# Kernel optimization log

Measured on AMD Instinct MI355X. Metric: run time of the kernel, lower is better.

Reference implementation:

```python
import jax, jax.numpy as jnp
import numpy as np

N, E, G = 8000, 100000, 256
H, C = 4, 128
ATOM_F = 92
L = 5


def _ln(x, g, b, eps=1e-5):
    mu = jnp.mean(x, axis=-1, keepdims=True)
    var = jnp.mean((x - mu) ** 2, axis=-1, keepdims=True)
    return (x - mu) * jax.lax.rsqrt(var + eps) * g + b


def setup_inputs() -> dict:
    key = jax.random.key(0)
    ks = iter(jax.random.split(key, 64))
    p = lambda shape: jax.random.normal(next(ks), shape, jnp.float32) * 0.05
    inp = {}
    inp['x'] = jax.random.normal(next(ks), (N, ATOM_F), jnp.float32)
    inp['edge_attr'] = jax.random.uniform(next(ks), (E,), jnp.float32)
    inp['edge_index'] = jax.random.randint(next(ks), (2, E), 0, N)
    inp['batch'] = jnp.sort(jax.random.randint(next(ks), (N,), 0, G))
    # atom embedding + rbf MLP
    inp['W_atom'] = p((ATOM_F, C)); inp['b_atom'] = jnp.zeros((C,))
    inp['W_rbf1'] = p((C, C)); inp['b_rbf1'] = jnp.zeros((C,))
    inp['W_rbf2'] = p((C, C)); inp['b_rbf2'] = jnp.zeros((C,))
    # 5 MatformerConv layers, params stacked on leading L dim
    inp['Wq'] = p((L, C, H * C)); inp['bq'] = jnp.zeros((L, H * C))
    inp['Wk'] = p((L, C, H * C)); inp['bk'] = jnp.zeros((L, H * C))
    inp['Wv'] = p((L, C, H * C)); inp['bv'] = jnp.zeros((L, H * C))
    inp['We'] = p((L, C, H * C))  # lin_edge has no bias
    inp['Wc'] = p((L, H * C, C)); inp['bc'] = jnp.zeros((L, C))
    inp['Wm'] = p((L, 3 * C, 3 * C)); inp['bm'] = jnp.zeros((L, 3 * C))
    inp['Wmsg'] = p((L, 3 * C, C)); inp['bmsg'] = jnp.zeros((L, C))
    inp['lnA_g'] = jnp.ones((L, 3 * C)); inp['lnA_b'] = jnp.zeros((L, 3 * C))
    inp['lnM_g'] = jnp.ones((L, C)); inp['lnM_b'] = jnp.zeros((L, C))
    inp['bn_g'] = jnp.ones((L, C)); inp['bn_b'] = jnp.zeros((L, C))
    inp['W_fc'] = p((C, C)); inp['b_fc'] = jnp.zeros((C,))
    return inp


def reference(x, edge_attr, edge_index, batch, W_atom, b_atom, W_rbf1, b_rbf1,
              W_rbf2, b_rbf2, Wq, bq, Wk, bk, Wv, bv, We, Wc, bc, Wm, bm,
              Wmsg, bmsg, lnA_g, lnA_b, lnM_g, lnM_b, bn_g, bn_b, W_fc, b_fc):
    n = x.shape[0]
    e_n = edge_attr.shape[0]
    src, dst = edge_index[0], edge_index[1]  # message flows src -> dst
    h = x @ W_atom + b_atom  # [N, C]
    # RBFExpansion(vmin=0, vmax=8, bins=128): gamma = 1/lengthscale
    centers = jnp.linspace(0.0, 8.0, C)
    gamma = (C - 1) / 8.0
    rbf = jnp.exp(-gamma * (edge_attr[:, None] - centers) ** 2)  # [E, C]
    ef = jax.nn.softplus(rbf @ W_rbf1 + b_rbf1) @ W_rbf2 + b_rbf2  # [E, C]
    scale = 1.0 / np.sqrt(3.0 * C).astype(np.float32)
    for l in range(L):
        q = (h @ Wq[l] + bq[l]).reshape(n, H, C)
        k = (h @ Wk[l] + bk[l]).reshape(n, H, C)
        v = (h @ Wv[l] + bv[l]).reshape(n, H, C)
        e = (ef @ We[l]).reshape(e_n, H, C)
        qi, ki, vi = q[dst], k[dst], v[dst]
        kj, vj = k[src], v[src]
        qc = jnp.concatenate([qi, qi, qi], axis=-1)           # [E, H, 3C]
        kc = jnp.concatenate([ki, kj, e], axis=-1)            # [E, H, 3C]
        alpha = qc * kc * scale
        gate = jax.nn.sigmoid(_ln(alpha, lnA_g[l], lnA_b[l]))
        m = jnp.concatenate([vi, vj, e], axis=-1) @ Wm[l] + bm[l]
        m = m * gate                                          # [E, H, 3C]
        m = _ln(m @ Wmsg[l] + bmsg[l], lnM_g[l], lnM_b[l])    # [E, H, C]
        agg = jax.ops.segment_sum(m.reshape(e_n, H * C), dst, num_segments=N)
        o = agg @ Wc[l] + bc[l]                               # [N, C]
        mu = jnp.mean(o, axis=0)
        var = jnp.mean((o - mu) ** 2, axis=0)                 # BatchNorm1d (train mode)
        o = (o - mu) * jax.lax.rsqrt(var + 1e-5) * bn_g[l] + bn_b[l]
        h = jax.nn.silu(o)
    counts = jax.ops.segment_sum(jnp.ones((n,), jnp.float32), batch, num_segments=G)
    pooled = jax.ops.segment_sum(h, batch, num_segments=G) / jnp.maximum(counts, 1.0)[:, None]
    return jax.nn.silu(pooled @ W_fc + b_fc)  # [G, 128]
```

## Files before the change

kernel.cpp:

```cpp
#include <hip/hip_runtime.h>
#include <math.h>

#define NN 8000
#define NE 100000
#define NG 256
#define CC 128
#define NH 4
#define HD 512
#define C3 384
#define HC3 1536
#define NL 5
#define AF 92
#define TE 16
#define TE2 32
#define NEB (NE/TE2)
#define SCALE 0.05103103630798288f

typedef __attribute__((ext_vector_type(8))) __bf16 bf16x8;
typedef __attribute__((ext_vector_type(4))) float f32x4;
typedef __attribute__((ext_vector_type(16))) float f32x16;
typedef __attribute__((ext_vector_type(8))) unsigned short us8;

static __device__ __forceinline__ bf16x8 ldbf8(const unsigned short* p){
  us8 v = *reinterpret_cast<const us8*>(p);
  return __builtin_bit_cast(bf16x8, v);
}
static __device__ __forceinline__ unsigned short f2bf(float f){
  unsigned int u = __builtin_bit_cast(unsigned int, f);
  u += 0x7FFFu + ((u >> 16) & 1u);
  return (unsigned short)(u >> 16);
}
static __device__ __forceinline__ float bf2f(unsigned short u){
  unsigned int x = ((unsigned int)u) << 16;
  return __builtin_bit_cast(float, x);
}
static __device__ __forceinline__ unsigned int packbf(float a, float b){
  return (unsigned int)f2bf(a) | ((unsigned int)f2bf(b) << 16);
}
static __device__ __forceinline__ float sigf(float x){ return 1.0f/(1.0f+__expf(-x)); }
static __device__ __forceinline__ float siluf(float x){ return x/(1.0f+__expf(-x)); }
static __device__ __forceinline__ float softplusf(float x){
  return x > 0.0f ? x + __logf(1.0f+__expf(-x)) : __logf(1.0f+__expf(x));
}
static __device__ __forceinline__ int permJ(int P){
  int tt = P >> 5;
  int r  = P & 31;
  int w  = tt / 3, part = tt - 3*w;
  return part*128 + w*32 + r;
}

__global__ void k_hist(const int* __restrict__ dstI, int* __restrict__ cnt){
  int i = blockIdx.x*256 + threadIdx.x;
  if (i < NE) atomicAdd(&cnt[dstI[i]], 1);
}
__global__ __launch_bounds__(1024)
void k_scan(const int* __restrict__ cnt, int* __restrict__ offs, int* __restrict__ cursor){
  __shared__ int a_s[1024], b_s[1024];
  int t = threadIdx.x;
  int base = t*8;
  int v[8]; int s = 0;
  #pragma unroll
  for (int j = 0; j < 8; ++j){
    int c = (base+j < NN) ? cnt[base+j] : 0;
    v[j] = s; s += c;
  }
  a_s[t] = s; __syncthreads();
  int* srcp = a_s; int* dstp = b_s;
  for (int off = 1; off < 1024; off <<= 1){
    int x = srcp[t];
    if (t >= off) x += srcp[t-off];
    dstp[t] = x; __syncthreads();
    int* tmp = srcp; srcp = dstp; dstp = tmp;
  }
  int excl = (t == 0) ? 0 : srcp[t-1];
  #pragma unroll
  for (int j = 0; j < 8; ++j){
    if (base+j < NN){ offs[base+j] = excl + v[j]; cursor[base+j] = excl + v[j]; }
  }
}
__global__ void k_scatter(const int* __restrict__ dstI, int* __restrict__ cursor,
                          int* __restrict__ sperm){
  int i = blockIdx.x*256 + threadIdx.x;
  if (i < NE){
    int d = dstI[i];
    int pos = atomicAdd(&cursor[d], 1);
    sperm[pos] = i;
  }
}
__global__ void k_meta(const int* __restrict__ sperm, const int* __restrict__ srcI,
                       const int* __restrict__ dstI, int* __restrict__ ssrc,
                       int* __restrict__ sdst){
  int i = blockIdx.x*256 + threadIdx.x;
  if (i < NE){ int e = sperm[i]; ssrc[i] = srcI[e]; sdst[i] = dstI[e]; }
}
__global__ void k_permute_ef(const int* __restrict__ sperm,
                             const uint2* __restrict__ ef_in, uint2* __restrict__ ef_out){
  int i = blockIdx.x*256 + threadIdx.x;
  if (i < NE*32){
    int row = i >> 5, p = i & 31;
    ef_out[(size_t)row*32 + p] = ef_in[(size_t)sperm[row]*32 + p];
  }
}

__global__ void k_prep_we(const float* __restrict__ We, unsigned short* __restrict__ WeA){
  size_t i = (size_t)blockIdx.x*256 + threadIdx.x;
  if (i >= (size_t)NL*NH*CC*CC) return;
  int k = i & 127; int r = (i>>7)&127; int hh = (i>>14)&3; int li = (int)(i>>16);
  WeA[i] = f2bf(We[((size_t)li*CC + k)*HD + hh*CC + r]);
}
__global__ void k_prep_wv(const float* __restrict__ Wm, unsigned short* __restrict__ WvA){
  size_t i = (size_t)blockIdx.x*256 + threadIdx.x;
  if (i >= (size_t)NL*768*CC) return;
  int k = i & 127; int R = (int)((i>>7) % 768); int li = (int)(i / (768*CC));
  int P = (R < C3) ? R : R - C3;
  int j = permJ(P);
  float val = (R < C3) ? Wm[((size_t)li*C3 + k)*C3 + j]
                       : Wm[((size_t)li*C3 + 128 + k)*C3 + j];
  WvA[i] = f2bf(val);
}
__global__ void k_prep_wg(const float* __restrict__ Wmsg, unsigned short* __restrict__ WgA){
  size_t i = (size_t)blockIdx.x*256 + threadIdx.x;
  if (i >= (size_t)NL*CC*C3) return;
  int P = (int)(i % C3); int c = (int)((i / C3) % CC); int li = (int)(i / ((size_t)CC*C3));
  WgA[i] = f2bf(Wmsg[((size_t)li*C3 + permJ(P))*CC + c]);
}
__global__ __launch_bounds__(128)
void k_prep_wf(const float* __restrict__ We, const float* __restrict__ Wm,
               unsigned short* __restrict__ WfA){
  int b = blockIdx.x;
  int P = b % C3; int hh = (b / C3) & 3; int li = b / (C3*NH);
  int o = permJ(P);
  __shared__ float wcol[CC];
  int t = threadIdx.x;
  wcol[t] = Wm[((size_t)li*C3 + 256 + t)*C3 + o];
  __syncthreads();
  const float* werow = We + ((size_t)li*CC + t)*HD + hh*CC;
  float acc = 0.f;
  #pragma unroll 4
  for (int c = 0; c < CC; ++c) acc += werow[c] * wcol[c];
  WfA[(((size_t)li*NH + hh)*C3 + P)*CC + t] = f2bf(acc);
}
__global__ void k_prep_wqkv(const float* __restrict__ Wq, const float* __restrict__ Wk,
                            const float* __restrict__ Wv, unsigned short* __restrict__ WA){
  size_t i = (size_t)blockIdx.x*256 + threadIdx.x;
  if (i >= (size_t)NL*1536*CC) return;
  int k = i & 127; int m = (int)((i>>7) % 1536); int li = (int)(i / ((size_t)1536*CC));
  const float* W = (m < 512) ? Wq : (m < 1024) ? Wk : Wv;
  int mm = m & 511;
  WA[i] = f2bf(W[((size_t)li*CC + k)*HD + mm]);
}
__global__ void k_prep_wc(const float* __restrict__ Wc, unsigned short* __restrict__ WcA){
  size_t i = (size_t)blockIdx.x*256 + threadIdx.x;
  if (i >= (size_t)NL*CC*HD) return;
  int k = (int)(i & 511); int r = (int)((i>>9) & 127); int li = (int)(i >> 16);
  WcA[i] = f2bf(Wc[((size_t)li*HD + k)*CC + r]);
}

__global__ __launch_bounds__(128)
void k_stem(const float* __restrict__ x, const float* __restrict__ W,
            const float* __restrict__ b, float* __restrict__ h,
            unsigned short* __restrict__ h_bf){
  __shared__ float xs[8][AF];
  int n0 = blockIdx.x*8;
  int t = threadIdx.x;
  for (int i = t; i < 8*AF; i += 128){ xs[i/AF][i%AF] = x[(size_t)n0*AF + i]; }
  __syncthreads();
  float acc[8] = {};
  for (int f = 0; f < AF; ++f){
    float w = W[f*CC + t];
    #pragma unroll
    for (int n = 0; n < 8; ++n) acc[n] += xs[n][f]*w;
  }
  float bb = b[t];
  #pragma unroll
  for (int n = 0; n < 8; ++n){
    float hv = acc[n] + bb;
    h[(size_t)(n0+n)*CC + t] = hv;
    h_bf[(size_t)(n0+n)*CC + t] = f2bf(hv);
  }
}

__global__ __launch_bounds__(128)
void k_rbf(const float* __restrict__ ea, const float* __restrict__ W1, const float* __restrict__ b1,
           const float* __restrict__ W2, const float* __restrict__ b2,
           unsigned short* __restrict__ ef){
  __shared__ __align__(16) float rs[8][CC];
  __shared__ __align__(16) float ss[8][CC];
  __shared__ float dv[8];
  int e0 = blockIdx.x*8; int t = threadIdx.x;
  if (t < 8) dv[t] = ea[e0 + t];
  __syncthreads();
  float center = (8.0f/127.0f) * (float)t;
  const float gamma = 15.875f;
  #pragma unroll
  for (int n = 0; n < 8; ++n){ float d = dv[n] - center; rs[n][t] = __expf(-gamma*d*d); }
  __syncthreads();
  {
    float acc[8] = {};
    for (int c0 = 0; c0 < CC; c0 += 4){
      float w0 = W1[(c0+0)*CC+t], w1 = W1[(c0+1)*CC+t], w2 = W1[(c0+2)*CC+t], w3 = W1[(c0+3)*CC+t];
      #pragma unroll
      for (int n = 0; n < 8; ++n){
        float4 r4 = *(const float4*)&rs[n][c0];
        acc[n] += r4.x*w0 + r4.y*w1 + r4.z*w2 + r4.w*w3;
      }
    }
    float bb = b1[t];
    #pragma unroll
    for (int n = 0; n < 8; ++n) ss[n][t] = softplusf(acc[n] + bb);
  }
  __syncthreads();
  {
    float acc[8] = {};
    for (int c0 = 0; c0 < CC; c0 += 4){
      float w0 = W2[(c0+0)*CC+t], w1 = W2[(c0+1)*CC+t], w2 = W2[(c0+2)*CC+t], w3 = W2[(c0+3)*CC+t];
      #pragma unroll
      for (int n = 0; n < 8; ++n){
        float4 r4 = *(const float4*)&ss[n][c0];
        acc[n] += r4.x*w0 + r4.y*w1 + r4.z*w2 + r4.w*w3;
      }
    }
    float bb = b2[t];
    #pragma unroll
    for (int n = 0; n < 8; ++n) ef[(size_t)(e0+n)*CC + t] = f2bf(acc[n] + bb);
  }
}

__global__ __launch_bounds__(256)
void k_qkv_mfma(const unsigned short* __restrict__ h_bf,
                const unsigned short* __restrict__ WA,
                const float* __restrict__ bq_, const float* __restrict__ bk_,
                const float* __restrict__ bv_,
                unsigned short* __restrict__ qo, unsigned short* __restrict__ ko,
                unsigned short* __restrict__ vo){
  const int t = threadIdx.x;
  const int w = t >> 6, lane = t & 63;
  const int col = lane & 31, hi = lane >> 5;
  const int node = blockIdx.x * 32 + col;
  const int yw = blockIdx.y;

  const unsigned short* hrow = h_bf + (size_t)node*CC + hi*8;
  bf16x8 bfr[8];
  #pragma unroll
  for (int kc = 0; kc < 8; ++kc) bfr[kc] = ldbf8(hrow + kc*16);

  const float* bias = (yw == 0) ? bq_ : (yw == 1) ? bk_ : bv_;
  unsigned short* outp = (yw == 0) ? qo : (yw == 1) ? ko : vo;
  const unsigned short* Wbase = WA + (size_t)yw*512*CC;

  #pragma unroll
  for (int mt = 0; mt < 4; ++mt){
    f32x16 acc;
    #pragma unroll
    for (int i = 0; i < 16; ++i) acc[i] = 0.f;
    const unsigned short* arow = Wbase + (size_t)(w*128 + mt*32 + col)*CC + hi*8;
    #pragma unroll
    for (int kc = 0; kc < 8; ++kc)
      acc = __builtin_amdgcn_mfma_f32_32x32x16_bf16(ldbf8(arow + kc*16), bfr[kc], acc, 0,0,0);
    #pragma unroll
    for (int g = 0; g < 4; ++g){
      int cb = w*128 + mt*32 + 8*g + 4*hi;
      float4 bb = *(const float4*)(bias + cb);
      uint2 uv;
      uv.x = packbf(acc[4*g+0]+bb.x, acc[4*g+1]+bb.y);
      uv.y = packbf(acc[4*g+2]+bb.z, acc[4*g+3]+bb.w);
      *(uint2*)(outp + (size_t)node*HD + cb) = uv;
    }
  }
}

__global__ __launch_bounds__(256)
void k_pv_mfma(const unsigned short* __restrict__ v_bf, const unsigned short* __restrict__ WvA,
               const float* __restrict__ bm,
               unsigned short* __restrict__ Pvi, unsigned short* __restrict__ Pvj){
  const int t = threadIdx.x;
  const int w = t >> 6, lane = t & 63;
  const int col = lane & 31, hi = lane >> 5;
  const int node = blockIdx.x * 32 + col;
  const int h = blockIdx.y;

  const unsigned short* vrow = v_bf + (size_t)node*HD + h*CC + hi*8;
  bf16x8 bfr[8];
  #pragma unroll
  for (int kc = 0; kc < 8; ++kc) bfr[kc] = ldbf8(vrow + kc*16);

  #pragma unroll
  for (int mt = 0; mt < 6; ++mt){
    f32x16 acc;
    #pragma unroll
    for (int i = 0; i < 16; ++i) acc[i] = 0.f;
    int R0 = w*192 + mt*32;
    const unsigned short* arow = WvA + (size_t)(R0 + col)*CC + hi*8;
    #pragma unroll
    for (int kc = 0; kc < 8; ++kc)
      acc = __builtin_amdgcn_mfma_f32_32x32x16_bf16(ldbf8(arow + kc*16), bfr[kc], acc, 0,0,0);
    if (R0 < C3){
      #pragma unroll
      for (int g = 0; g < 4; ++g){
        int P0 = R0 + 8*g + 4*hi;
        int j0 = permJ(P0);
        float4 bq = *(const float4*)(bm + j0);
        uint2 uv;
        uv.x = packbf(acc[4*g+0]+bq.x, acc[4*g+1]+bq.y);
        uv.y = packbf(acc[4*g+2]+bq.z, acc[4*g+3]+bq.w);
        *(uint2*)(Pvi + (size_t)node*HC3 + h*C3 + P0) = uv;
      }
    } else {
      #pragma unroll
      for (int g = 0; g < 4; ++g){
        int P0 = R0 - C3 + 8*g + 4*hi;
        uint2 uv;
        uv.x = packbf(acc[4*g+0], acc[4*g+1]);
        uv.y = packbf(acc[4*g+2], acc[4*g+3]);
        *(uint2*)(Pvj + (size_t)node*HC3 + h*C3 + P0) = uv;
      }
    }
  }
}

__global__ __launch_bounds__(256, 3)
void k_edge_mfma(const unsigned short* __restrict__ ef_bf,
                 const unsigned short* __restrict__ q_bf, const unsigned short* __restrict__ k_bf,
                 const unsigned short* __restrict__ Pvi, const unsigned short* __restrict__ Pvj,
                 const int* __restrict__ ssrc, const int* __restrict__ sdst,
                 const unsigned short* __restrict__ WeA,
                 const unsigned short* __restrict__ WfA,
                 const unsigned short* __restrict__ WgA,
                 const float* __restrict__ lnAg, const float* __restrict__ lnAb,
                 const float* __restrict__ lnMg, const float* __restrict__ lnMb,
                 const float* __restrict__ bmsg,
                 float* __restrict__ agg)
{
  __shared__ __align__(16) union {
    unsigned short m[TE2][392];
    float mf[TE2][132];
  } u_s;
  __shared__ float red1[4][TE2][2];
  __shared__ float red2[4][TE2][2];
  __shared__ int sdst_s[TE2];

  const int t = threadIdx.x;
  const int w = t >> 6, lane = t & 63;
  const int col = lane & 31, hi = lane >> 5;
  const int e0 = blockIdx.x * TE2;
  const int h  = blockIdx.y;
  const int edge = e0 + col;
  const int dst = sdst[edge], src = ssrc[edge];
  if (t < TE2) sdst_s[t] = sdst[e0 + t];

  const unsigned short* efrow = ef_bf + (size_t)edge*CC + hi*8;
  bf16x8 bfr[8];
  #pragma unroll
  for (int kc = 0; kc < 8; ++kc) bfr[kc] = ldbf8(efrow + kc*16);

  ushort4 q4[4], kd4[4], kj4[4];
  #pragma unroll
  for (int g = 0; g < 4; ++g){
    int c0 = w*32 + 8*g + 4*hi;
    q4[g]  = *(const ushort4*)(q_bf + (size_t)dst*HD + h*CC + c0);
    kd4[g] = *(const ushort4*)(k_bf + (size_t)dst*HD + h*CC + c0);
    kj4[g] = *(const ushort4*)(k_bf + (size_t)src*HD + h*CC + c0);
  }

  const unsigned short* WeAh = WeA + (size_t)h*CC*CC;
  f32x16 acc1;
  #pragma unroll
  for (int i = 0; i < 16; ++i) acc1[i] = 0.f;
  {
    const unsigned short* arow = WeAh + (size_t)(w*32 + col)*CC + hi*8;
    #pragma unroll
    for (int kc = 0; kc < 8; ++kc)
      acc1 = __builtin_amdgcn_mfma_f32_32x32x16_bf16(ldbf8(arow + kc*16), bfr[kc], acc1, 0,0,0);
  }

  float av[48];
  float s1 = 0.f, s2 = 0.f;
  #pragma unroll
  for (int reg = 0; reg < 16; ++reg){
    int g = reg >> 2, i = reg & 3;
    float qv  = bf2f(((const unsigned short*)&q4[g])[i]);
    float kdv = bf2f(((const unsigned short*)&kd4[g])[i]);
    float kjv = bf2f(((const unsigned short*)&kj4[g])[i]);
    float x0 = qv*kdv;
    float x1 = qv*kjv;
    float x2 = qv*acc1[reg];
    av[reg] = x0; av[16+reg] = x1; av[32+reg] = x2;
    s1 += x0+x1+x2;
    s2 += x0*x0+x1*x1+x2*x2;
  }
  s1 += __shfl_xor(s1, 32); s2 += __shfl_xor(s2, 32);
  if (hi == 0){ red1[w][col][0] = s1; red1[w][col][1] = s2; }
  __syncthreads();

  ushort4 pi4[12], pj4[12];
  #pragma unroll
  for (int part = 0; part < 3; ++part){
    #pragma unroll
    for (int g = 0; g < 4; ++g){
      int P0 = w*96 + part*32 + 8*g + 4*hi;
      pi4[part*4+g] = *(const ushort4*)(Pvi + (size_t)dst*HC3 + h*C3 + P0);
      pj4[part*4+g] = *(const ushort4*)(Pvj + (size_t)src*HC3 + h*C3 + P0);
    }
  }

  {
    float S1 = red1[0][col][0] + red1[1][col][0] + red1[2][col][0] + red1[3][col][0];
    float S2 = red1[0][col][1] + red1[1][col][1] + red1[2][col][1] + red1[3][col][1];
    float mu = S1 * (1.0f/384.0f);
    float var = S2 * (1.0f/384.0f) - mu*mu;
    float coef = SCALE * rsqrtf(SCALE*SCALE*var + 1e-5f);
    #pragma unroll
    for (int part = 0; part < 3; ++part){
      #pragma unroll
      for (int g = 0; g < 4; ++g){
        int j0 = part*128 + w*32 + 8*g + 4*hi;
        float4 gg = *(const float4*)(lnAg + j0);
        float4 bb = *(const float4*)(lnAb + j0);
        av[part*16+4*g+0] = sigf((av[part*16+4*g+0]-mu)*coef*gg.x + bb.x);
        av[part*16+4*g+1] = sigf((av[part*16+4*g+1]-mu)*coef*gg.y + bb.y);
        av[part*16+4*g+2] = sigf((av[part*16+4*g+2]-mu)*coef*gg.z + bb.z);
        av[part*16+4*g+3] = sigf((av[part*16+4*g+3]-mu)*coef*gg.w + bb.w);
      }
    }
  }

  const unsigned short* WfAh = WfA + (size_t)h*C3*CC;
  #pragma unroll
  for (int part = 0; part < 3; ++part){
    f32x16 acc2;
    #pragma unroll
    for (int i = 0; i < 16; ++i) acc2[i] = 0.f;
    const unsigned short* arow = WfAh + (size_t)(w*96 + part*32 + col)*CC + hi*8;
    #pragma unroll
    for (int kc = 0; kc < 8; ++kc)
      acc2 = __builtin_amdgcn_mfma_f32_32x32x16_bf16(ldbf8(arow + kc*16), bfr[kc], acc2, 0,0,0);
    #pragma unroll
    for (int g = 0; g < 4; ++g){
      float m0 = (acc2[4*g+0] + bf2f(pi4[part*4+g].x) + bf2f(pj4[part*4+g].x)) * av[part*16+4*g+0];
      float m1 = (acc2[4*g+1] + bf2f(pi4[part*4+g].y) + bf2f(pj4[part*4+g].y)) * av[part*16+4*g+1];
      float m2 = (acc2[4*g+2] + bf2f(pi4[part*4+g].z) + bf2f(pj4[part*4+g].z)) * av[part*16+4*g+2];
      float m3 = (acc2[4*g+3] + bf2f(pi4[part*4+g].w) + bf2f(pj4[part*4+g].w)) * av[part*16+4*g+3];
      uint2 uv;
      uv.x = packbf(m0, m1);
      uv.y = packbf(m2, m3);
      *(uint2*)&u_s.m[col][w*96 + part*32 + 8*g + 4*hi] = uv;
    }
  }
  __syncthreads();

  f32x16 acc3;
  #pragma unroll
  for (int i = 0; i < 16; ++i) acc3[i] = 0.f;
  {
    const unsigned short* arow = WgA + (size_t)(w*32 + col)*C3 + hi*8;
    #pragma unroll
    for (int kc = 0; kc < 24; ++kc)
      acc3 = __builtin_amdgcn_mfma_f32_32x32x16_bf16(ldbf8(arow + kc*16),
                                                     ldbf8(&u_s.m[col][kc*16 + hi*8]), acc3, 0,0,0);
  }
  float vals[16];
  {
    float t1 = 0.f, t2 = 0.f;
    #pragma unroll
    for (int g = 0; g < 4; ++g){
      float4 bq = *(const float4*)(bmsg + w*32 + 8*g + 4*hi);
      float v0 = acc3[4*g+0] + bq.x; float v1 = acc3[4*g+1] + bq.y;
      float v2 = acc3[4*g+2] + bq.z; float v3 = acc3[4*g+3] + bq.w;
      vals[4*g+0]=v0; vals[4*g+1]=v1; vals[4*g+2]=v2; vals[4*g+3]=v3;
      t1 += v0+v1+v2+v3; t2 += v0*v0+v1*v1+v2*v2+v3*v3;
    }
    t1 += __shfl_xor(t1, 32); t2 += __shfl_xor(t2, 32);
    if (hi == 0){ red2[w][col][0] = t1; red2[w][col][1] = t2; }
  }
  __syncthreads();
  {
    float S1 = red2[0][col][0] + red2[1][col][0] + red2[2][col][0] + red2[3][col][0];
    float S2 = red2[0][col][1] + red2[1][col][1] + red2[2][col][1] + red2[3][col][1];
    float mu = S1 * (1.0f/128.0f);
    float inv = rsqrtf(S2 * (1.0f/128.0f) - mu*mu + 1e-5f);
    #pragma unroll
    for (int g = 0; g < 4; ++g){
      int c0 = w*32 + 8*g + 4*hi;
      float4 gg = *(const float4*)(lnMg + c0);
      float4 bb = *(const float4*)(lnMb + c0);
      float4 r;
      r.x = (vals[4*g+0] - mu)*inv*gg.x + bb.x;
      r.y = (vals[4*g+1] - mu)*inv*gg.y + bb.y;
      r.z = (vals[4*g+2] - mu)*inv*gg.z + bb.z;
      r.w = (vals[4*g+3] - mu)*inv*gg.w + bb.w;
      *(float4*)&u_s.mf[col][c0] = r;
    }
  }
  __syncthreads();
  {
    int c = t & 127, grp = t >> 7;
    int base = grp*16;
    float run = 0.f;
    int d0 = sdst_s[base];
    #pragma unroll 4
    for (int e2 = base; e2 < base + 16; ++e2){
      int d = sdst_s[e2];
      if (d != d0){
        atomicAdd(agg + (size_t)d0*HD + h*CC + c, run);
        run = 0.f; d0 = d;
      }
      run += u_s.mf[e2][c];
    }
    atomicAdd(agg + (size_t)d0*HD + h*CC + c, run);
  }
}

__global__ __launch_bounds__(256)
void k_oc(const float* __restrict__ agg, const unsigned short* __restrict__ WcA,
          const float* __restrict__ bc, float* __restrict__ o, float* __restrict__ bns){
  const int t = threadIdx.x;
  const int wv = t >> 6, l = t & 63;
  const int lr = l & 15, lg = l >> 4;
  const int node = blockIdx.x*TE + lr;

  const float* arow_ = agg + (size_t)node*HD + lg*8;
  f32x4 acc[2]; acc[0] = f32x4{0.f,0.f,0.f,0.f}; acc[1] = f32x4{0.f,0.f,0.f,0.f};
  for (int ks = 0; ks < 16; ++ks){
    float fbuf[8];
    *(float4*)&fbuf[0] = *(const float4*)(arow_ + ks*32);
    *(float4*)&fbuf[4] = *(const float4*)(arow_ + ks*32 + 4);
    us8 hv, lv;
    #pragma unroll
    for (int i = 0; i < 8; ++i){
      float f = fbuf[i];
      unsigned int u = __builtin_bit_cast(unsigned int, f);
      hv[i] = (unsigned short)(u >> 16);
      float hf = __builtin_bit_cast(float, u & 0xFFFF0000u);
      lv[i] = f2bf(f - hf);
    }
    bf16x8 bhi = __builtin_bit_cast(bf16x8, hv);
    bf16x8 blo = __builtin_bit_cast(bf16x8, lv);
    #pragma unroll
    for (int mt = 0; mt < 2; ++mt){
      bf16x8 a = ldbf8(WcA + (size_t)(wv*32 + mt*16 + lr)*HD + ks*32 + lg*8);
      acc[mt] = __builtin_amdgcn_mfma_f32_16x16x32_bf16(a, bhi, acc[mt], 0,0,0);
      acc[mt] = __builtin_amdgcn_mfma_f32_16x16x32_bf16(a, blo, acc[mt], 0,0,0);
    }
  }
  #pragma unroll
  for (int mt = 0; mt < 2; ++mt){
    int c0 = wv*32 + mt*16 + lg*4;
    float4 bb = *(const float4*)(bc + c0);
    float4 ov;
    ov.x = acc[mt][0]+bb.x; ov.y = acc[mt][1]+bb.y; ov.z = acc[mt][2]+bb.z; ov.w = acc[mt][3]+bb.w;
    *(float4*)(o + (size_t)node*CC + c0) = ov;
    float vv[4] = {ov.x, ov.y, ov.z, ov.w};
    #pragma unroll
    for (int r = 0; r < 4; ++r){
      float a = vv[r], b = vv[r]*vv[r];
      a += __shfl_xor(a, 1); b += __shfl_xor(b, 1);
      a += __shfl_xor(a, 2); b += __shfl_xor(b, 2);
      a += __shfl_xor(a, 4); b += __shfl_xor(b, 4);
      a += __shfl_xor(a, 8); b += __shfl_xor(b, 8);
      if (lr == 0){ atomicAdd(&bns[c0+r], a); atomicAdd(&bns[CC+c0+r], b); }
    }
  }
}

__global__ void k_bnsilu(const float* __restrict__ o, const float* __restrict__ bns,
                         const float* __restrict__ g, const float* __restrict__ b,
                         float* __restrict__ h, unsigned short* __restrict__ h_bf){
  int i = blockIdx.x*256 + threadIdx.x;
  if (i < NN*CC){
    int c = i & 127;
    float mu = bns[c] * (1.0f/NN);
    float inv = rsqrtf(bns[CC+c] * (1.0f/NN) - mu*mu + 1e-5f);
    float z = (o[i] - mu) * inv * g[c] + b[c];
    float hv = siluf(z);
    h[i] = hv;
    h_bf[i] = f2bf(hv);
  }
}

__global__ void k_pool(const float* __restrict__ h, const int* __restrict__ batch,
                       float* __restrict__ pooled, float* __restrict__ counts){
  int i = blockIdx.x*256 + threadIdx.x;
  if (i < NN*CC){
    int n = i >> 7, c = i & 127;
    int g = batch[n];
    atomicAdd(&pooled[g*CC + c], h[i]);
    if (c == 0) atomicAdd(&counts[g], 1.0f);
  }
}

__global__ __launch_bounds__(128)
void k_final(const float* __restrict__ pooled, const float* __restrict__ counts,
             const float* __restrict__ Wfc, const float* __restrict__ bfc,
             float* __restrict__ out){
  __shared__ float psh[CC];
  int g = blockIdx.x; int t = threadIdx.x;
  float rc = 1.0f / fmaxf(counts[g], 1.0f);
  psh[t] = pooled[g*CC + t] * rc;
  __syncthreads();
  float acc = 0.f;
  for (int c = 0; c < CC; ++c) acc += psh[c] * Wfc[c*CC + t];
  out[g*CC + t] = siluf(acc + bfc[t]);
}

extern "C" void kernel_launch(void* const* d_in, const int* in_sizes, int n_in,
                              void* d_out, int out_size, void* d_ws, size_t ws_size,
                              hipStream_t stream){
  const float* x      = (const float*)d_in[0];
  const float* ea     = (const float*)d_in[1];
  const int*   ei     = (const int*)d_in[2];
  const int*   batch  = (const int*)d_in[3];
  const float* W_atom = (const float*)d_in[4];  const float* b_atom = (const float*)d_in[5];
  const float* W_rbf1 = (const float*)d_in[6];  const float* b_rbf1 = (const float*)d_in[7];
  const float* W_rbf2 = (const float*)d_in[8];  const float* b_rbf2 = (const float*)d_in[9];
  const float* Wq     = (const float*)d_in[10]; const float* bq     = (const float*)d_in[11];
  const float* Wk     = (const float*)d_in[12]; const float* bk     = (const float*)d_in[13];
  const float* Wv     = (const float*)d_in[14]; const float* bv     = (const float*)d_in[15];
  const float* We     = (const float*)d_in[16];
  const float* Wc     = (const float*)d_in[17]; const float* bc     = (const float*)d_in[18];
  const float* Wm     = (const float*)d_in[19]; const float* bm     = (const float*)d_in[20];
  const float* Wmsg   = (const float*)d_in[21]; const float* bmsg   = (const float*)d_in[22];
  const float* lnAg   = (const float*)d_in[23]; const float* lnAb   = (const float*)d_in[24];
  const float* lnMg   = (const float*)d_in[25]; const float* lnMb   = (const float*)d_in[26];
  const float* bng    = (const float*)d_in[27]; const float* bnb    = (const float*)d_in[28];
  const float* Wfc    = (const float*)d_in[29]; const float* bfc    = (const float*)d_in[30];

  float* ws = (float*)d_ws;
  size_t off = 0;
  auto alloc = [&](size_t n){ float* p = ws + off; off += n; return p; };
  float* h      = alloc((size_t)NN*CC);
  float* o      = alloc((size_t)NN*CC);
  float* agg    = alloc((size_t)NN*HD);
  unsigned short* h_bf  = (unsigned short*)alloc((size_t)NN*CC/2);
  unsigned short* qb_bf = (unsigned short*)alloc((size_t)NN*HD/2);
  unsigned short* kb_bf = (unsigned short*)alloc((size_t)NN*HD/2);
  unsigned short* vb_bf = (unsigned short*)alloc((size_t)NN*HD/2);
  unsigned short* Pvi   = (unsigned short*)alloc((size_t)NN*HC3/2);
  unsigned short* Pvj   = (unsigned short*)alloc((size_t)NN*HC3/2);
  unsigned short* ef_bf = (unsigned short*)alloc((size_t)NE*CC/2);
  unsigned short* efs_bf= (unsigned short*)alloc((size_t)NE*CC/2);
  unsigned short* WeA   = (unsigned short*)alloc((size_t)NL*NH*CC*CC/2);
  unsigned short* WfA   = (unsigned short*)alloc((size_t)NL*NH*C3*CC/2);
  unsigned short* WvA   = (unsigned short*)alloc((size_t)NL*768*CC/2);
  unsigned short* WgA   = (unsigned short*)alloc((size_t)NL*CC*C3/2);
  unsigned short* WqkvA = (unsigned short*)alloc((size_t)NL*1536*CC/2);
  unsigned short* WcA   = (unsigned short*)alloc((size_t)NL*CC*HD/2);
  int* cnt    = (int*)alloc(8192);
  int* offs   = (int*)alloc(NN);
  int* cursor = (int*)alloc(NN);
  int* sperm  = (int*)alloc(NE);
  int* ssrc   = (int*)alloc(NE);
  int* sdst   = (int*)alloc(NE);
  float* bns    = alloc(2*CC);
  float* pooled = alloc((size_t)NG*CC);
  float* counts = alloc(NG);

  if (off * sizeof(float) > ws_size){
    hipMemsetAsync(d_out, 0x7F, (size_t)out_size*sizeof(float), stream);
    return;
  }

  const int* srcI = ei;
  const int* dstI = ei + NE;

  hipMemsetAsync(cnt, 0, 8192*sizeof(int), stream);
  k_hist<<<(NE+255)/256, 256, 0, stream>>>(dstI, cnt);
  k_scan<<<1, 1024, 0, stream>>>(cnt, offs, cursor);
  k_scatter<<<(NE+255)/256, 256, 0, stream>>>(dstI, cursor, sperm);
  k_meta<<<(NE+255)/256, 256, 0, stream>>>(sperm, srcI, dstI, ssrc, sdst);

  k_prep_we<<<(NL*NH*CC*CC + 255)/256, 256, 0, stream>>>(We, WeA);
  k_prep_wv<<<(NL*768*CC + 255)/256, 256, 0, stream>>>(Wm, WvA);
  k_prep_wg<<<(NL*CC*C3 + 255)/256, 256, 0, stream>>>(Wmsg, WgA);
  k_prep_wf<<<NL*NH*C3, 128, 0, stream>>>(We, Wm, WfA);
  k_prep_wqkv<<<(NL*1536*CC + 255)/256, 256, 0, stream>>>(Wq, Wk, Wv, WqkvA);
  k_prep_wc<<<(NL*CC*HD + 255)/256, 256, 0, stream>>>(Wc, WcA);

  k_stem<<<NN/8, 128, 0, stream>>>(x, W_atom, b_atom, h, h_bf);
  k_rbf<<<NE/8, 128, 0, stream>>>(ea, W_rbf1, b_rbf1, W_rbf2, b_rbf2, ef_bf);
  k_permute_ef<<<(NE*32 + 255)/256, 256, 0, stream>>>(sperm, (const uint2*)ef_bf, (uint2*)efs_bf);

  for (int l = 0; l < NL; ++l){
    const float* bq_l   = bq   + (size_t)l*HD;
    const float* bk_l   = bk   + (size_t)l*HD;
    const float* bv_l   = bv   + (size_t)l*HD;
    const float* bc_l   = bc   + (size_t)l*CC;
    const float* bm_l   = bm   + (size_t)l*C3;
    const float* bmsg_l = bmsg + (size_t)l*CC;
    const float* lnAg_l = lnAg + (size_t)l*C3;      const float* lnAb_l = lnAb + (size_t)l*C3;
    const float* lnMg_l = lnMg + (size_t)l*CC;      const float* lnMb_l = lnMb + (size_t)l*CC;
    const float* bng_l  = bng  + (size_t)l*CC;      const float* bnb_l  = bnb  + (size_t)l*CC;
    const unsigned short* WeA_l = WeA + (size_t)l*NH*CC*CC;
    const unsigned short* WfA_l = WfA + (size_t)l*NH*C3*CC;
    const unsigned short* WvA_l = WvA + (size_t)l*768*CC;
    const unsigned short* WgA_l = WgA + (size_t)l*CC*C3;
    const unsigned short* WqkvA_l = WqkvA + (size_t)l*1536*CC;
    const unsigned short* WcA_l = WcA + (size_t)l*CC*HD;

    k_qkv_mfma<<<dim3(NN/32, 3), 256, 0, stream>>>(h_bf, WqkvA_l, bq_l, bk_l, bv_l,
                                                   qb_bf, kb_bf, vb_bf);
    k_pv_mfma<<<dim3(NN/32, NH), 256, 0, stream>>>(vb_bf, WvA_l, bm_l, Pvi, Pvj);

    hipMemsetAsync(agg, 0, (size_t)NN*HD*sizeof(float), stream);
    hipMemsetAsync(bns, 0, 2*CC*sizeof(float), stream);

    k_edge_mfma<<<dim3(NEB, NH), 256, 0, stream>>>(efs_bf, qb_bf, kb_bf, Pvi, Pvj, ssrc, sdst,
                                                   WeA_l, WfA_l, WgA_l,
                                                   lnAg_l, lnAb_l, lnMg_l, lnMb_l, bmsg_l, agg);

    k_oc<<<NN/TE, 256, 0, stream>>>(agg, WcA_l, bc_l, o, bns);
    k_bnsilu<<<(NN*CC+255)/256, 256, 0, stream>>>(o, bns, bng_l, bnb_l, h, h_bf);
  }

  hipMemsetAsync(pooled, 0, ((size_t)NG*CC + NG)*sizeof(float), stream);
  k_pool<<<(NN*CC+255)/256, 256, 0, stream>>>(h, batch, pooled, counts);
  k_final<<<NG, 128, 0, stream>>>(pooled, counts, Wfc, bfc, (float*)d_out);
}
```

Before: 3.668 ms.

## Fuse edge-feature permutation into RBF kernel, add MFMA setprio, merge memsets

The scatter kernel now also records each edge's sorted position, so the RBF MLP writes its bf16 edge features straight into sorted order. This removes the separate permute kernel and the intermediate buffer. MFMA loops across the GEMM and edge kernels are wrapped in s_setprio to raise wave priority during matrix work. The bns buffer is moved next to agg so one memset per layer clears both. The RBF stores become scattered rows rather than contiguous ones.

```diff
diff --git a/kernel.cpp b/kernel.cpp
--- a/kernel.cpp
+++ b/kernel.cpp
@@ -79,12 +79,13 @@
   }
 }
 __global__ void k_scatter(const int* __restrict__ dstI, int* __restrict__ cursor,
-                          int* __restrict__ sperm){
+                          int* __restrict__ sperm, int* __restrict__ iperm){
   int i = blockIdx.x*256 + threadIdx.x;
   if (i < NE){
     int d = dstI[i];
     int pos = atomicAdd(&cursor[d], 1);
     sperm[pos] = i;
+    iperm[i] = pos;
   }
 }
 __global__ void k_meta(const int* __restrict__ sperm, const int* __restrict__ srcI,
@@ -92,14 +93,6 @@
                        int* __restrict__ sdst){
   int i = blockIdx.x*256 + threadIdx.x;
   if (i < NE){ int e = sperm[i]; ssrc[i] = srcI[e]; sdst[i] = dstI[e]; }
-}
-__global__ void k_permute_ef(const int* __restrict__ sperm,
-                             const uint2* __restrict__ ef_in, uint2* __restrict__ ef_out){
-  int i = blockIdx.x*256 + threadIdx.x;
-  if (i < NE*32){
-    int row = i >> 5, p = i & 31;
-    ef_out[(size_t)row*32 + p] = ef_in[(size_t)sperm[row]*32 + p];
-  }
 }
 
 __global__ void k_prep_we(const float* __restrict__ We, unsigned short* __restrict__ WeA){
@@ -183,12 +176,13 @@
 __global__ __launch_bounds__(128)
 void k_rbf(const float* __restrict__ ea, const float* __restrict__ W1, const float* __restrict__ b1,
            const float* __restrict__ W2, const float* __restrict__ b2,
-           unsigned short* __restrict__ ef){
+           const int* __restrict__ iperm, unsigned short* __restrict__ efs){
   __shared__ __align__(16) float rs[8][CC];
   __shared__ __align__(16) float ss[8][CC];
   __shared__ float dv[8];
+  __shared__ int ip_s[8];
   int e0 = blockIdx.x*8; int t = threadIdx.x;
-  if (t < 8) dv[t] = ea[e0 + t];
+  if (t < 8){ dv[t] = ea[e0 + t]; ip_s[t] = iperm[e0 + t]; }
   __syncthreads();
   float center = (8.0f/127.0f) * (float)t;
   const float gamma = 15.875f;
@@ -222,7 +216,7 @@
     }
     float bb = b2[t];
     #pragma unroll
-    for (int n = 0; n < 8; ++n) ef[(size_t)(e0+n)*CC + t] = f2bf(acc[n] + bb);
+    for (int n = 0; n < 8; ++n) efs[(size_t)ip_s[n]*CC + t] = f2bf(acc[n] + bb);
   }
 }
 
@@ -254,9 +248,11 @@
     #pragma unroll
     for (int i = 0; i < 16; ++i) acc[i] = 0.f;
     const unsigned short* arow = Wbase + (size_t)(w*128 + mt*32 + col)*CC + hi*8;
+    __builtin_amdgcn_s_setprio(1);
     #pragma unroll
     for (int kc = 0; kc < 8; ++kc)
       acc = __builtin_amdgcn_mfma_f32_32x32x16_bf16(ldbf8(arow + kc*16), bfr[kc], acc, 0,0,0);
+    __builtin_amdgcn_s_setprio(0);
     #pragma unroll
     for (int g = 0; g < 4; ++g){
       int cb = w*128 + mt*32 + 8*g + 4*hi;
@@ -291,9 +287,11 @@
     for (int i = 0; i < 16; ++i) acc[i] = 0.f;
     int R0 = w*192 + mt*32;
     const unsigned short* arow = WvA + (size_t)(R0 + col)*CC + hi*8;
+    __builtin_amdgcn_s_setprio(1);
     #pragma unroll
     for (int kc = 0; kc < 8; ++kc)
       acc = __builtin_amdgcn_mfma_f32_32x32x16_bf16(ldbf8(arow + kc*16), bfr[kc], acc, 0,0,0);
+    __builtin_amdgcn_s_setprio(0);
     if (R0 < C3){
       #pragma unroll
       for (int g = 0; g < 4; ++g){
@@ -368,9 +366,11 @@
   for (int i = 0; i < 16; ++i) acc1[i] = 0.f;
   {
     const unsigned short* arow = WeAh + (size_t)(w*32 + col)*CC + hi*8;
+    __builtin_amdgcn_s_setprio(1);
     #pragma unroll
     for (int kc = 0; kc < 8; ++kc)
       acc1 = __builtin_amdgcn_mfma_f32_32x32x16_bf16(ldbf8(arow + kc*16), bfr[kc], acc1, 0,0,0);
+    __builtin_amdgcn_s_setprio(0);
   }
 
   float av[48];
@@ -431,9 +431,11 @@
     #pragma unroll
     for (int i = 0; i < 16; ++i) acc2[i] = 0.f;
     const unsigned short* arow = WfAh + (size_t)(w*96 + part*32 + col)*CC + hi*8;
+    __builtin_amdgcn_s_setprio(1);
     #pragma unroll
     for (int kc = 0; kc < 8; ++kc)
       acc2 = __builtin_amdgcn_mfma_f32_32x32x16_bf16(ldbf8(arow + kc*16), bfr[kc], acc2, 0,0,0);
+    __builtin_amdgcn_s_setprio(0);
     #pragma unroll
     for (int g = 0; g < 4; ++g){
       float m0 = (acc2[4*g+0] + bf2f(pi4[part*4+g].x) + bf2f(pj4[part*4+g].x)) * av[part*16+4*g+0];
@@ -453,10 +455,12 @@
   for (int i = 0; i < 16; ++i) acc3[i] = 0.f;
   {
     const unsigned short* arow = WgA + (size_t)(w*32 + col)*C3 + hi*8;
+    __builtin_amdgcn_s_setprio(1);
     #pragma unroll
     for (int kc = 0; kc < 24; ++kc)
       acc3 = __builtin_amdgcn_mfma_f32_32x32x16_bf16(ldbf8(arow + kc*16),
                                                      ldbf8(&u_s.m[col][kc*16 + hi*8]), acc3, 0,0,0);
+    __builtin_amdgcn_s_setprio(0);
   }
   float vals[16];
   {
@@ -535,12 +539,14 @@
     }
     bf16x8 bhi = __builtin_bit_cast(bf16x8, hv);
     bf16x8 blo = __builtin_bit_cast(bf16x8, lv);
+    __builtin_amdgcn_s_setprio(1);
     #pragma unroll
     for (int mt = 0; mt < 2; ++mt){
       bf16x8 a = ldbf8(WcA + (size_t)(wv*32 + mt*16 + lr)*HD + ks*32 + lg*8);
       acc[mt] = __builtin_amdgcn_mfma_f32_16x16x32_bf16(a, bhi, acc[mt], 0,0,0);
       acc[mt] = __builtin_amdgcn_mfma_f32_16x16x32_bf16(a, blo, acc[mt], 0,0,0);
     }
+    __builtin_amdgcn_s_setprio(0);
   }
   #pragma unroll
   for (int mt = 0; mt < 2; ++mt){
@@ -630,13 +636,13 @@
   float* h      = alloc((size_t)NN*CC);
   float* o      = alloc((size_t)NN*CC);
   float* agg    = alloc((size_t)NN*HD);
+  float* bns    = alloc(2*CC);
   unsigned short* h_bf  = (unsigned short*)alloc((size_t)NN*CC/2);
   unsigned short* qb_bf = (unsigned short*)alloc((size_t)NN*HD/2);
   unsigned short* kb_bf = (unsigned short*)alloc((size_t)NN*HD/2);
   unsigned short* vb_bf = (unsigned short*)alloc((size_t)NN*HD/2);
   unsigned short* Pvi   = (unsigned short*)alloc((size_t)NN*HC3/2);
   unsigned short* Pvj   = (unsigned short*)alloc((size_t)NN*HC3/2);
-  unsigned short* ef_bf = (unsigned short*)alloc((size_t)NE*CC/2);
   unsigned short* efs_bf= (unsigned short*)alloc((size_t)NE*CC/2);
   unsigned short* WeA   = (unsigned short*)alloc((size_t)NL*NH*CC*CC/2);
   unsigned short* WfA   = (unsigned short*)alloc((size_t)NL*NH*C3*CC/2);
@@ -648,9 +654,9 @@
   int* offs   = (int*)alloc(NN);
   int* cursor = (int*)alloc(NN);
   int* sperm  = (int*)alloc(NE);
+  int* iperm  = (int*)alloc(NE);
   int* ssrc   = (int*)alloc(NE);
   int* sdst   = (int*)alloc(NE);
-  float* bns    = alloc(2*CC);
   float* pooled = alloc((size_t)NG*CC);
   float* counts = alloc(NG);
 
@@ -665,7 +671,7 @@
   hipMemsetAsync(cnt, 0, 8192*sizeof(int), stream);
   k_hist<<<(NE+255)/256, 256, 0, stream>>>(dstI, cnt);
   k_scan<<<1, 1024, 0, stream>>>(cnt, offs, cursor);
-  k_scatter<<<(NE+255)/256, 256, 0, stream>>>(dstI, cursor, sperm);
+  k_scatter<<<(NE+255)/256, 256, 0, stream>>>(dstI, cursor, sperm, iperm);
   k_meta<<<(NE+255)/256, 256, 0, stream>>>(sperm, srcI, dstI, ssrc, sdst);
 
   k_prep_we<<<(NL*NH*CC*CC + 255)/256, 256, 0, stream>>>(We, WeA);
@@ -676,8 +682,7 @@
   k_prep_wc<<<(NL*CC*HD + 255)/256, 256, 0, stream>>>(Wc, WcA);
 
   k_stem<<<NN/8, 128, 0, stream>>>(x, W_atom, b_atom, h, h_bf);
-  k_rbf<<<NE/8, 128, 0, stream>>>(ea, W_rbf1, b_rbf1, W_rbf2, b_rbf2, ef_bf);
-  k_permute_ef<<<(NE*32 + 255)/256, 256, 0, stream>>>(sperm, (const uint2*)ef_bf, (uint2*)efs_bf);
+  k_rbf<<<NE/8, 128, 0, stream>>>(ea, W_rbf1, b_rbf1, W_rbf2, b_rbf2, iperm, efs_bf);
 
   for (int l = 0; l < NL; ++l){
     const float* bq_l   = bq   + (size_t)l*HD;
@@ -700,8 +705,7 @@
                                                    qb_bf, kb_bf, vb_bf);
     k_pv_mfma<<<dim3(NN/32, NH), 256, 0, stream>>>(vb_bf, WvA_l, bm_l, Pvi, Pvj);
 
-    hipMemsetAsync(agg, 0, (size_t)NN*HD*sizeof(float), stream);
-    hipMemsetAsync(bns, 0, 2*CC*sizeof(float), stream);
+    hipMemsetAsync(agg, 0, ((size_t)NN*HD + 2*CC)*sizeof(float), stream);
 
     k_edge_mfma<<<dim3(NEB, NH), 256, 0, stream>>>(efs_bf, qb_bf, kb_bf, Pvi, Pvj, ssrc, sdst,
                                                    WeA_l, WfA_l, WgA_l,
```

Measured after the change: 3.806 ms. 1.04x slower.
